# Optimization experiments

Hardware: AMD Instinct MI355X
Metric: run time of the kernel (lower is better)

The kernel has to match this reference:

```python
import jax, jax.numpy as jnp
import numpy as np

# Problem dims: batch B, n variables, m constraints (from A_shape=(512,256))
B, N, M_CON = 64, 256, 512
# OSQP ADMM hyper-parameters (standard OSQP defaults: sigma, rho, relaxation alpha)
SIGMA, RHO, ALPHA = 1e-6, 0.1, 1.6
ITERS = 200  # fixed iteration count (max_iter) for jit-compatibility


def setup_inputs() -> dict:
    key = jax.random.key(0)
    k1, k2, k3, k4, k5 = jax.random.split(key, 5)
    # Diagonal PSD P: strictly positive diagonal values
    P_val = jax.random.uniform(k1, (B, N), dtype=jnp.float32) + 0.1
    q_val = jax.random.normal(k2, (B, N), dtype=jnp.float32)
    # Dense A, row-major flattened [m*n]; scaled for conditioning
    A_val = jax.random.normal(k3, (B, M_CON * N), dtype=jnp.float32) * 0.1
    # Bounds with l < 0 < u roughly (x=0 feasible -> QP always solvable)
    c = jax.random.normal(k4, (B, M_CON), dtype=jnp.float32)
    w = jax.random.uniform(k5, (B, M_CON), dtype=jnp.float32)
    l_val = c - w - 0.1
    u_val = c + w + 0.1
    return {"P_val": P_val, "q_val": q_val, "A_val": A_val,
            "l_val": l_val, "u_val": u_val}


def _cho_solve(L, rhs):
    # batched lower-triangular Cholesky solve: M x = rhs, M = L L^T
    y = jax.scipy.linalg.solve_triangular(L, rhs[..., None], lower=True)
    x = jax.scipy.linalg.solve_triangular(jnp.swapaxes(L, -1, -2), y, lower=False)
    return x[..., 0]


def _osqp_admm(P_diag, q, A, l, u):
    """Batched OSQP ADMM: min 1/2 x'Px + q'x  s.t. l <= Ax <= u.
    P is diagonal (P_diag per-item diagonal). Returns primal solution x [B, n]."""
    n = q.shape[-1]
    # KKT-condensed matrix: M = P + sigma*I + rho*A'A, Cholesky-factored once.
    Mmat = jax.vmap(jnp.diag)(P_diag) + SIGMA * jnp.eye(n, dtype=q.dtype) \
        + RHO * jnp.einsum('bmi,bmj->bij', A, A)
    L = jnp.linalg.cholesky(Mmat)

    def step(carry, _):
        x, z, y = carry
        rhs = SIGMA * x - q + jnp.einsum('bmn,bm->bn', A, RHO * z - y)
        x_tilde = _cho_solve(L, rhs)                  # [B, n]
        z_tilde = jnp.einsum('bmn,bn->bm', A, x_tilde)  # [B, m]
        x_new = ALPHA * x_tilde + (1.0 - ALPHA) * x
        z_relax = ALPHA * z_tilde + (1.0 - ALPHA) * z
        z_new = jnp.clip(z_relax + y / RHO, l, u)     # projection onto [l, u]
        y_new = y + RHO * (z_relax - z_new)
        return (x_new, z_new, y_new), None

    init = (jnp.zeros_like(q), jnp.zeros_like(l), jnp.zeros_like(l))
    (x, _, _), _ = jax.lax.scan(step, init, None, length=ITERS)
    return x


def reference(P_val, q_val, A_val, l_val, u_val):
    A = A_val.reshape(B, M_CON, N)
    return _osqp_admm(P_val, q_val, A, l_val, u_val)
```

## Files before the change

### kernel.cpp

```cpp
#include <hip/hip_runtime.h>
#include <hip/hip_fp16.h>

#define B_      64
#define N_      256
#define M_      512
#define SIGMA_  1e-6f
#define RHO_    0.1f
#define ALPHA_  1.6f
#define BETA_   (-0.6f)
#define ITERS_  200

#if defined(__has_builtin)
#if __has_builtin(__builtin_amdgcn_fdot2)
#define HAVE_FDOT2 1
#endif
#endif

typedef _Float16 h2_t __attribute__((ext_vector_type(2)));

__device__ __forceinline__ float fdot2f(__half2 a, __half2 b, float c) {
#ifdef HAVE_FDOT2
    return __builtin_amdgcn_fdot2(__builtin_bit_cast(h2_t, a),
                                  __builtin_bit_cast(h2_t, b), c, false);
#else
    return c + __low2float(a) * __low2float(b) + __high2float(a) * __high2float(b);
#endif
}

__device__ __forceinline__ float fdot2u(unsigned int a, unsigned int b, float c) {
    return fdot2f(__builtin_bit_cast(__half2, a), __builtin_bit_cast(__half2, b), c);
}

__device__ __forceinline__ unsigned short bf16rne(float f) {
    unsigned int u = __builtin_bit_cast(unsigned int, f);
    u += 0x7fffu + ((u >> 16) & 1u);
    return (unsigned short)(u >> 16);
}
__device__ __forceinline__ float bf16tof(unsigned short h) {
    unsigned int u = ((unsigned int)h) << 16;
    return __builtin_bit_cast(float, u);
}

__device__ __forceinline__ float f4c(const float4& v, int k) {
    return k == 0 ? v.x : k == 1 ? v.y : k == 2 ? v.z : v.w;
}

__global__ __launch_bounds__(256) void gemm_bt(
    const float* __restrict__ Af, const __half* __restrict__ Ah, int lda, long long sA, int tA,
    const float* __restrict__ Bf, int ldb, long long sB, int tB,
    const float* __restrict__ Dp, int ldd, long long sD,
    float* __restrict__ Cf, __half* __restrict__ Ch, int ldc, long long sC,
    float alpha, float beta, int Mx, int Nx, int Kx, int packPairs,
    float* __restrict__ Gdr, long long sGdr)
{
    __shared__ float as_[16][68];
    __shared__ float bs_[16][68];

    const int tid = threadIdx.x;
    const int b   = blockIdx.z;
    const int i0  = blockIdx.y * 64;
    const int j0  = blockIdx.x * 64;

    if (Af) Af += (size_t)b * sA;
    if (Ah) Ah += (size_t)b * sA;
    Bf += (size_t)b * sB;
    if (Dp) Dp += (size_t)b * sD;
    if (Cf) Cf += (size_t)b * sC;
    if (Ch) Ch += (size_t)b * sC;
    if (Gdr) Gdr += (size_t)b * sGdr;

    const int ty = tid >> 4;
    const int tx = tid & 15;

    float acc[4][4] = {};

    #pragma unroll 1
    for (int k0 = 0; k0 < Kx; k0 += 16) {
        if (tA) {
            const int kk = tid >> 4, i4 = (tid & 15) << 2;
            float4 v = *(const float4*)(Af + (size_t)(k0 + kk) * lda + i0 + i4);
            *(float4*)&as_[kk][i4] = v;
        } else {
            const int ii = tid >> 2, k4 = (tid & 3) << 2;
            if (Ah) {
                const __half2* hp = (const __half2*)(Ah + (size_t)(i0 + ii) * lda + k0 + k4);
                __half2 h0 = hp[0], h1 = hp[1];
                as_[k4 + 0][ii] = __low2float(h0);
                as_[k4 + 1][ii] = __high2float(h0);
                as_[k4 + 2][ii] = __low2float(h1);
                as_[k4 + 3][ii] = __high2float(h1);
            } else {
                float4 v = *(const float4*)(Af + (size_t)(i0 + ii) * lda + k0 + k4);
                as_[k4 + 0][ii] = v.x; as_[k4 + 1][ii] = v.y;
                as_[k4 + 2][ii] = v.z; as_[k4 + 3][ii] = v.w;
            }
        }
        if (tB) {
            const int jj = tid >> 2, k4 = (tid & 3) << 2;
            float4 v = *(const float4*)(Bf + (size_t)(j0 + jj) * ldb + k0 + k4);
            bs_[k4 + 0][jj] = v.x; bs_[k4 + 1][jj] = v.y;
            bs_[k4 + 2][jj] = v.z; bs_[k4 + 3][jj] = v.w;
        } else {
            const int kk = tid >> 4, j4 = (tid & 15) << 2;
            float4 v = *(const float4*)(Bf + (size_t)(k0 + kk) * ldb + j0 + j4);
            *(float4*)&bs_[kk][j4] = v;
        }
        __syncthreads();

        #pragma unroll
        for (int kk = 0; kk < 16; kk++) {
            float4 av = *(float4*)&as_[kk][ty << 2];
            float4 bv = *(float4*)&bs_[kk][tx << 2];
            acc[0][0] += av.x * bv.x; acc[0][1] += av.x * bv.y;
            acc[0][2] += av.x * bv.z; acc[0][3] += av.x * bv.w;
            acc[1][0] += av.y * bv.x; acc[1][1] += av.y * bv.y;
            acc[1][2] += av.y * bv.z; acc[1][3] += av.y * bv.w;
            acc[2][0] += av.z * bv.x; acc[2][1] += av.z * bv.y;
            acc[2][2] += av.z * bv.z; acc[2][3] += av.z * bv.w;
            acc[3][0] += av.w * bv.x; acc[3][1] += av.w * bv.y;
            acc[3][2] += av.w * bv.z; acc[3][3] += av.w * bv.w;
        }
        __syncthreads();
    }

    if (Ch) {
        if (packPairs) {
            __half2* C2 = (__half2*)Ch;
            const int mrow = i0 + (ty << 2);
            #pragma unroll
            for (int p = 0; p < 2; p++) {
                #pragma unroll
                for (int jj = 0; jj < 4; jj++) {
                    const float v0 = alpha * acc[2 * p][jj];
                    const float v1 = alpha * acc[2 * p + 1][jj];
                    __half2 h = __floats2half2_rn(v0, v1);
                    C2[(size_t)((mrow >> 1) + p) * ldc + j0 + (tx << 2) + jj] = h;
                    if (Gdr) {
                        const int col = j0 + (tx << 2) + jj;
                        const int r0  = mrow + 2 * p;
                        if (col == r0)          Gdr[col] = v0 - __low2float(h);
                        else if (col == r0 + 1) Gdr[col] = v1 - __high2float(h);
                    }
                }
            }
        } else {
            #pragma unroll
            for (int ii = 0; ii < 4; ii++) {
                #pragma unroll
                for (int jj = 0; jj < 4; jj++) {
                    Ch[(size_t)(i0 + (ty << 2) + ii) * ldc + j0 + (tx << 2) + jj] =
                        __float2half_rn(alpha * acc[ii][jj]);
                }
            }
        }
    } else {
        #pragma unroll
        for (int ii = 0; ii < 4; ii++) {
            const int m = i0 + (ty << 2) + ii;
            const int n = j0 + (tx << 2);
            float4 v;
            v.x = alpha * acc[ii][0]; v.y = alpha * acc[ii][1];
            v.z = alpha * acc[ii][2]; v.w = alpha * acc[ii][3];
            if (Dp) {
                float4 d = *(const float4*)(Dp + (size_t)m * ldd + n);
                v.x += beta * d.x; v.y += beta * d.y;
                v.z += beta * d.z; v.w += beta * d.w;
            }
            *(float4*)(Cf + (size_t)m * ldc + n) = v;
        }
    }
}

typedef __attribute__((ext_vector_type(8))) short bfrag;
typedef __attribute__((ext_vector_type(4))) float ffrag;

__global__ __launch_bounds__(256) void mfma_nt(
    const unsigned short* __restrict__ Xh, const unsigned short* __restrict__ Xl,
    const unsigned short* __restrict__ Yh, const unsigned short* __restrict__ Yl,
    int Kx, long long sX, long long sY,
    void* __restrict__ out0, void* __restrict__ out1,
    int ldc, long long sC, long long sC2, int mode,
    const float* __restrict__ Pd, float alpha)
{
    __shared__ unsigned short Ysh[2][64][264];

    const int tid = threadIdx.x;
    const int w   = tid >> 6;
    const int l   = tid & 63;
    const int b   = blockIdx.z;
    const int rowbase = blockIdx.y * 64 + w * 16;
    const int colbase = blockIdx.x * 64;
    const int lr = l & 15;
    const int q  = l >> 4;

    const unsigned short* xh = Xh + (size_t)b * sX + (size_t)(rowbase + lr) * Kx + q * 8;
    const unsigned short* xl = Xl + (size_t)b * sX + (size_t)(rowbase + lr) * Kx + q * 8;
    const unsigned short* ybh = Yh + (size_t)b * sY;
    const unsigned short* ybl = Yl + (size_t)b * sY;

    ffrag acc[4] = {};

    #pragma unroll 1
    for (int kc = 0; kc < Kx; kc += 256) {
        __syncthreads();
        #pragma unroll
        for (int e = 0; e < 8; e++) {
            const int idx = e * 256 + tid;
            const int c  = idx >> 5;
            const int kq = idx & 31;
            const size_t so = (size_t)(colbase + c) * Kx + kc + kq * 8;
            *(uint4*)&Ysh[0][c][kq * 8] = *(const uint4*)(ybh + so);
            *(uint4*)&Ysh[1][c][kq * 8] = *(const uint4*)(ybl + so);
        }
        __syncthreads();

        #pragma unroll 2
        for (int k0 = kc; k0 < kc + 256; k0 += 32) {
            bfrag ah = *(const bfrag*)(xh + k0);
            bfrag al = *(const bfrag*)(xl + k0);
            const int ko = (k0 - kc) + q * 8;
            #pragma unroll
            for (int t = 0; t < 4; t++) {
                bfrag bh = *(const bfrag*)&Ysh[0][16 * t + lr][ko];
                bfrag bl = *(const bfrag*)&Ysh[1][16 * t + lr][ko];
                acc[t] = __builtin_amdgcn_mfma_f32_16x16x32_bf16(ah, bh, acc[t], 0, 0, 0);
                acc[t] = __builtin_amdgcn_mfma_f32_16x16x32_bf16(ah, bl, acc[t], 0, 0, 0);
                acc[t] = __builtin_amdgcn_mfma_f32_16x16x32_bf16(al, bh, acc[t], 0, 0, 0);
            }
        }
    }

    if (mode == 0) {
        float* Cf = (float*)out0 + (size_t)b * sC;
        #pragma unroll
        for (int t = 0; t < 4; t++) {
            #pragma unroll
            for (int p = 0; p < 4; p++) {
                const int r  = rowbase + q * 4 + p;
                const int cc = colbase + 16 * t + lr;
                float v = alpha * acc[t][p];
                if (Pd && cc == r) v += Pd[b * 256 + r] + SIGMA_;
                Cf[(size_t)r * ldc + cc] = v;
            }
        }
    } else if (mode == 1) {
        unsigned short* Fh = (unsigned short*)out0 + (size_t)b * sC;
        unsigned short* Fl = (unsigned short*)out1 + (size_t)b * sC;
        #pragma unroll
        for (int t = 0; t < 4; t++) {
            #pragma unroll
            for (int p = 0; p < 4; p++) {
                const int r  = rowbase + q * 4 + p;
                const int cc = colbase + 16 * t + lr;
                const float v = acc[t][p];
                const unsigned short hh = bf16rne(v);
                Fh[(size_t)r * ldc + cc] = hh;
                Fl[(size_t)r * ldc + cc] = bf16rne(v - bf16tof(hh));
            }
        }
    } else {
        unsigned int* Gpp = (unsigned int*)out0 + (size_t)b * sC;
        float* Gd = (float*)out1 + (size_t)b * sC2;
        #pragma unroll
        for (int t = 0; t < 4; t++) {
            #pragma unroll
            for (int p2 = 0; p2 < 2; p2++) {
                const int r0 = rowbase + q * 4 + 2 * p2;
                const int cc = colbase + 16 * t + lr;
                const float v0 = acc[t][2 * p2], v1 = acc[t][2 * p2 + 1];
                __half2 h = __floats2half2_rn(v0, v1);
                Gpp[(size_t)(r0 >> 1) * ldc + cc] = __builtin_bit_cast(unsigned int, h);
                if (cc == r0)          Gd[cc] = v0 - __low2float(h);
                else if (cc == r0 + 1) Gd[cc] = v1 - __high2float(h);
            }
        }
    }
}

__global__ __launch_bounds__(256) void prep_a(
    const float* __restrict__ A, unsigned short* __restrict__ Th,
    unsigned short* __restrict__ Tl, unsigned short* __restrict__ Ahh,
    unsigned short* __restrict__ All)
{
    __shared__ float t_[64][65];
    const int b  = blockIdx.z;
    const int r0 = blockIdx.x * 64;
    const int c0 = blockIdx.y * 64;
    const int tid = threadIdx.x;
    const int ty = tid >> 4, tx = tid & 15;
    const float* Ab = A + (size_t)b * 131072;
    unsigned short* Ahb = Ahh + (size_t)b * 131072;
    unsigned short* Alb = All + (size_t)b * 131072;

    #pragma unroll
    for (int p = 0; p < 4; p++) {
        const int rr = ty + p * 16;
        const size_t o = (size_t)(r0 + rr) * 256 + c0 + tx * 4;
        float4 v = *(const float4*)(Ab + o);
        t_[rr][tx * 4 + 0] = v.x; t_[rr][tx * 4 + 1] = v.y;
        t_[rr][tx * 4 + 2] = v.z; t_[rr][tx * 4 + 3] = v.w;
        unsigned short h0 = bf16rne(v.x), h1 = bf16rne(v.y);
        unsigned short h2 = bf16rne(v.z), h3 = bf16rne(v.w);
        uint2 hp, lp;
        hp.x = (unsigned int)h0 | ((unsigned int)h1 << 16);
        hp.y = (unsigned int)h2 | ((unsigned int)h3 << 16);
        lp.x = (unsigned int)bf16rne(v.x - bf16tof(h0)) |
               ((unsigned int)bf16rne(v.y - bf16tof(h1)) << 16);
        lp.y = (unsigned int)bf16rne(v.z - bf16tof(h2)) |
               ((unsigned int)bf16rne(v.w - bf16tof(h3)) << 16);
        *(uint2*)(Ahb + o) = hp;
        *(uint2*)(Alb + o) = lp;
    }
    __syncthreads();

    unsigned short* Thb = Th + (size_t)b * 131072;
    unsigned short* Tlb = Tl + (size_t)b * 131072;
    #pragma unroll
    for (int p = 0; p < 4; p++) {
        const int ar = ty + p * 16;
        unsigned int hp[2], lp[2];
        #pragma unroll
        for (int d2 = 0; d2 < 2; d2++) {
            unsigned short h0, h1, l0, l1;
            {
                const float v = t_[tx * 4 + 2 * d2][ar];
                h0 = bf16rne(v); l0 = bf16rne(v - bf16tof(h0));
            }
            {
                const float v = t_[tx * 4 + 2 * d2 + 1][ar];
                h1 = bf16rne(v); l1 = bf16rne(v - bf16tof(h1));
            }
            hp[d2] = (unsigned int)h0 | ((unsigned int)h1 << 16);
            lp[d2] = (unsigned int)l0 | ((unsigned int)l1 << 16);
        }
        const size_t o = (size_t)(c0 + ar) * 512 + r0 + tx * 4;
        *(uint2*)(Thb + o) = make_uint2(hp[0], hp[1]);
        *(uint2*)(Tlb + o) = make_uint2(lp[0], lp[1]);
    }
}

__global__ void add_diag(float* __restrict__ Mm, const float* __restrict__ P)
{
    const int b = blockIdx.x, t = threadIdx.x;
    Mm[(size_t)b * 65536 + (size_t)t * 257] += P[b * 256 + t] + SIGMA_;
}

__device__ __forceinline__ int gja(int i, int j)
{
    return (i << 7) + ((((j >> 2) ^ (i & 31)) << 2) | (j & 3));
}
__device__ __forceinline__ float4 ldsq(const float* Mp, int row, int q)
{
    return *(const float4*)&Mp[(row << 7) + (((q ^ (row & 31)) << 2))];
}
__device__ __forceinline__ void stsq(float* Mp, int row, int q, float4 v)
{
    *(float4*)&Mp[(row << 7) + (((q ^ (row & 31)) << 2))] = v;
}

__device__ void gj_lds(float* Msh, float (&Dsh)[16][17], float (&CT)[16][136],
                       float (&RS)[16][136], float (&CDs)[16][136],
                       float (&rowB)[2][16], float (&colB)[2][16], float (&pB)[2],
                       int tid)
{
    const int di = tid >> 4;
    const int dj = tid & 15;

    #pragma unroll 1
    for (int t = 0; t < 8; t++) {
        const int tb = t << 4;

        float a = Msh[gja(tb + di, tb + dj)];
        #pragma unroll
        for (int g2 = 0; g2 < 2; g2++) {
            const int i0 = (dj << 2) + (g2 << 6);
            float4 cv;
            if ((i0 >> 4) == t) {
                cv.x = 0.f; cv.y = 0.f; cv.z = 0.f; cv.w = 0.f;
            } else {
                cv.x = Msh[gja(i0 + 0, tb + di)];
                cv.y = Msh[gja(i0 + 1, tb + di)];
                cv.z = Msh[gja(i0 + 2, tb + di)];
                cv.w = Msh[gja(i0 + 3, tb + di)];
            }
            *(float4*)&CT[di][i0] = cv;
        }
        __syncthreads();

        #pragma unroll 1
        for (int k = 0; k < 16; k++) {
            const int kb = k & 1;
            if (dj == k) colB[kb][di] = a;
            if (di == k) {
                rowB[kb][dj] = a;
                if (dj == k) pB[kb] = 1.0f / a;
            }
            __syncthreads();
            const float ip = pB[kb];
            const float rj = rowB[kb][dj];
            const float ci = colB[kb][di];
            if (di == k)      a = (dj == k) ? ip : rj * ip;
            else if (dj == k) a = -ci * ip;
            else              a -= ci * (rj * ip);
        }
        Dsh[di][dj] = a;
        __syncthreads();

        #pragma unroll
        for (int g2 = 0; g2 < 2; g2++) {
            const int j = (dj << 2) + (g2 << 6);
            float4 s; s.x = 0.f; s.y = 0.f; s.z = 0.f; s.w = 0.f;
            if ((j >> 4) != t) {
                #pragma unroll
                for (int m = 0; m < 16; m++) {
                    const float d = Dsh[di][m];
                    const float4 rv = ldsq(Msh, tb + m, j >> 2);
                    s.x += d * rv.x; s.y += d * rv.y;
                    s.z += d * rv.z; s.w += d * rv.w;
                }
            }
            *(float4*)&RS[di][j] = s;

            float4 sc; sc.x = 0.f; sc.y = 0.f; sc.z = 0.f; sc.w = 0.f;
            #pragma unroll
            for (int m = 0; m < 16; m++) {
                const float d = Dsh[m][di];
                const float4 cv = *(const float4*)&CT[m][j];
                sc.x += d * cv.x; sc.y += d * cv.y;
                sc.z += d * cv.z; sc.w += d * cv.w;
            }
            *(float4*)&CDs[di][j] = sc;
        }
        __syncthreads();

        {
            const int ty = di, tx = dj;
            float4 v0[8], v1[8];
            int cofs0[8], cofs1[8];
            #pragma unroll
            for (int r = 0; r < 8; r++) {
                const int i = (ty << 3) + r;
                const int e = i & 31;
                const int base = i << 7;
                cofs0[r] = base + ((((tx << 1)     ) ^ e) << 2);
                cofs1[r] = base + ((((tx << 1) | 1 ) ^ e) << 2);
                v0[r] = *(float4*)&Msh[cofs0[r]];
                v1[r] = *(float4*)&Msh[cofs1[r]];
            }
            #pragma unroll 1
            for (int k = 0; k < 16; k++) {
                const float4 r0 = *(const float4*)&RS[k][tx << 3];
                const float4 r1 = *(const float4*)&RS[k][(tx << 3) + 4];
                const float4 c0 = *(const float4*)&CT[k][ty << 3];
                const float4 c1 = *(const float4*)&CT[k][(ty << 3) + 4];
                const float cc[8] = {c0.x, c0.y, c0.z, c0.w,
                                     c1.x, c1.y, c1.z, c1.w};
                #pragma unroll
                for (int r = 0; r < 8; r++) {
                    const float c = cc[r];
                    v0[r].x -= c * r0.x; v0[r].y -= c * r0.y;
                    v0[r].z -= c * r0.z; v0[r].w -= c * r0.w;
                    v1[r].x -= c * r1.x; v1[r].y -= c * r1.y;
                    v1[r].z -= c * r1.z; v1[r].w -= c * r1.w;
                }
            }
            #pragma unroll
            for (int r = 0; r < 8; r++) {
                *(float4*)&Msh[cofs0[r]] = v0[r];
                *(float4*)&Msh[cofs1[r]] = v1[r];
            }
        }
        __syncthreads();

        #pragma unroll
        for (int g2 = 0; g2 < 2; g2++) {
            const int j = (dj << 2) + (g2 << 6);
            if ((j >> 4) != t) {
                stsq(Msh, tb + di, j >> 2, *(const float4*)&RS[di][j]);
                const float4 cd = *(const float4*)&CDs[di][j];
                Msh[gja(j + 0, tb + di)] = -cd.x;
                Msh[gja(j + 1, tb + di)] = -cd.y;
                Msh[gja(j + 2, tb + di)] = -cd.z;
                Msh[gja(j + 3, tb + di)] = -cd.w;
            }
        }
        Msh[gja(tb + di, tb + dj)] = Dsh[di][dj];
        __syncthreads();
    }
}

__global__ __launch_bounds__(256) void gj128_blk(
    const float* __restrict__ src, int lsrc, long long ssrc,
    float* __restrict__ dst, int ldst, long long sdst)
{
    extern __shared__ float Msh[];
    __shared__ float Dsh[16][17];
    __shared__ float CT[16][136];
    __shared__ float RS[16][136];
    __shared__ float CDs[16][136];
    __shared__ float rowB[2][16], colB[2][16], pB[2];

    const int tid = threadIdx.x, b = blockIdx.x;
    src += (size_t)b * ssrc;
    dst += (size_t)b * sdst;

    for (int qd = 0; qd < 64; qd++) {
        const int idx = qd * 256 + tid;
        const int i = idx >> 7, j = idx & 127;
        Msh[gja(i, j)] = src[(size_t)i * lsrc + j];
    }
    __syncthreads();
    gj_lds(Msh, Dsh, CT, RS, CDs, rowB, colB, pB, tid);
    for (int qd = 0; qd < 64; qd++) {
        const int idx = qd * 256 + tid;
        const int i = idx >> 7, j = idx & 127;
        dst[(size_t)i * ldst + j] = Msh[gja(i, j)];
    }
}

__global__ __launch_bounds__(256) void schur_inv(
    const float* __restrict__ Mmat, float* __restrict__ Ebuf,
    float* __restrict__ Minv, unsigned short* __restrict__ Mh,
    unsigned short* __restrict__ Ml)
{
    __shared__ float A1[16384];
    __shared__ float A2[16384];
    __shared__ float Dsh[16][17];
    __shared__ float CT[16][136];
    __shared__ float RS[16][136];
    __shared__ float CDs[16][136];
    __shared__ float rowB[2][16], colB[2][16], pB[2];

    const int tid = threadIdx.x, b = blockIdx.x;
    const float* Mb = Mmat + (size_t)b * 65536;
    float* Eb = Ebuf + (size_t)b * 16384;
    float* Ib = Minv + (size_t)b * 65536;
    unsigned short* Mhb = Mh + (size_t)b * 65536;
    unsigned short* Mlb = Ml + (size_t)b * 65536;

    const int ty = tid >> 4, tx = tid & 15;

    for (int qd = 0; qd < 64; qd++) {
        const int idx = qd * 256 + tid;
        const int i = idx >> 7, j = idx & 127;
        A1[gja(i, j)] = Mb[(size_t)i * 256 + j];
    }
    __syncthreads();
    gj_lds(A1, Dsh, CT, RS, CDs, rowB, colB, pB, tid);

    for (int qd = 0; qd < 64; qd++) {
        const int idx = qd * 256 + tid;
        const int i = idx >> 7, j = idx & 127;
        Eb[(size_t)i * 128 + j] = A1[gja(i, j)];
        A2[gja(i, j)] = Mb[(size_t)(128 + i) * 256 + j];
    }
    __syncthreads();

    {
        float acc[8][8] = {};
        #pragma unroll 1
        for (int k4 = 0; k4 < 32; k4++) {
            float4 mq[8];
            #pragma unroll
            for (int r = 0; r < 8; r++) mq[r] = ldsq(A2, 8 * ty + r, k4);
            #pragma unroll
            for (int kk = 0; kk < 4; kk++) {
                const int k = k4 * 4 + kk;
                const float4 e0 = ldsq(A1, k, 2 * tx);
                const float4 e1 = ldsq(A1, k, 2 * tx + 1);
                const float ev[8] = {e0.x, e0.y, e0.z, e0.w, e1.x, e1.y, e1.z, e1.w};
                #pragma unroll
                for (int r = 0; r < 8; r++) {
                    const float m = f4c(mq[r], kk);
                    #pragma unroll
                    for (int c = 0; c < 8; c++) acc[r][c] += m * ev[c];
                }
            }
        }
        __syncthreads();
        #pragma unroll
        for (int r = 0; r < 8; r++) {
            float4 o0, o1;
            o0.x = acc[r][0]; o0.y = acc[r][1]; o0.z = acc[r][2]; o0.w = acc[r][3];
            o1.x = acc[r][4]; o1.y = acc[r][5]; o1.z = acc[r][6]; o1.w = acc[r][7];
            stsq(A2, 8 * ty + r, 2 * tx, o0);
            stsq(A2, 8 * ty + r, 2 * tx + 1, o1);
        }
        __syncthreads();
    }

    {
        float acc[8][8];
        #pragma unroll
        for (int r = 0; r < 8; r++) {
            const float4 a0 = *(const float4*)&Mb[(size_t)(128 + 8 * ty + r) * 256 + 128 + 8 * tx];
            const float4 a1 = *(const float4*)&Mb[(size_t)(128 + 8 * ty + r) * 256 + 128 + 8 * tx + 4];
            acc[r][0] = a0.x; acc[r][1] = a0.y; acc[r][2] = a0.z; acc[r][3] = a0.w;
            acc[r][4] = a1.x; acc[r][5] = a1.y; acc[r][6] = a1.z; acc[r][7] = a1.w;
        }
        #pragma unroll 1
        for (int kt = 0; kt < 8; kt++) {
            __syncthreads();
            #pragma unroll
            for (int e = 0; e < 8; e++) {
                const int idx = e * 256 + tid;
                const int kk = idx >> 7, j = idx & 127;
                RS[kk][j] = Mb[(size_t)(kt * 16 + kk) * 256 + 128 + j];
            }
            __syncthreads();
            #pragma unroll 1
            for (int k2 = 0; k2 < 16; k2 += 4) {
                const int kq = (kt * 16 + k2) >> 2;
                float4 tq[8];
                #pragma unroll
                for (int r = 0; r < 8; r++) tq[r] = ldsq(A2, 8 * ty + r, kq);
                #pragma unroll
                for (int kk = 0; kk < 4; kk++) {
                    const float4 m0 = *(const float4*)&RS[k2 + kk][8 * tx];
                    const float4 m1 = *(const float4*)&RS[k2 + kk][8 * tx + 4];
                    const float mv[8] = {m0.x, m0.y, m0.z, m0.w, m1.x, m1.y, m1.z, m1.w};
                    #pragma unroll
                    for (int r = 0; r < 8; r++) {
                        const float t2 = f4c(tq[r], kk);
                        #pragma unroll
                        for (int c = 0; c < 8; c++) acc[r][c] -= t2 * mv[c];
                    }
                }
            }
        }
        __syncthreads();
        #pragma unroll
        for (int r = 0; r < 8; r++) {
            float4 o0, o1;
            o0.x = acc[r][0]; o0.y = acc[r][1]; o0.z = acc[r][2]; o0.w = acc[r][3];
            o1.x = acc[r][4]; o1.y = acc[r][5]; o1.z = acc[r][6]; o1.w = acc[r][7];
            stsq(A1, 8 * ty + r, 2 * tx, o0);
            stsq(A1, 8 * ty + r, 2 * tx + 1, o1);
        }
        __syncthreads();
    }

    gj_lds(A1, Dsh, CT, RS, CDs, rowB, colB, pB, tid);
    for (int qd = 0; qd < 64; qd++) {
        const int idx = qd * 256 + tid;
        const int i = idx >> 7, j = idx & 127;
        const float v = A1[gja(i, j)];
        const size_t o = (size_t)(128 + i) * 256 + 128 + j;
        Ib[o] = v;
        const unsigned short hh = bf16rne(v);
        Mhb[o] = hh; Mlb[o] = bf16rne(v - bf16tof(hh));
    }

    {
        float acc[8][8] = {};
        #pragma unroll 1
        for (int k4 = 0; k4 < 32; k4++) {
            float4 sq[8];
            #pragma unroll
            for (int r = 0; r < 8; r++) sq[r] = ldsq(A1, 8 * ty + r, k4);
            #pragma unroll
            for (int kk = 0; kk < 4; kk++) {
                const int k = k4 * 4 + kk;
                const float4 t0 = ldsq(A2, k, 2 * tx);
                const float4 t1 = ldsq(A2, k, 2 * tx + 1);
                const float tv[8] = {t0.x, t0.y, t0.z, t0.w, t1.x, t1.y, t1.z, t1.w};
                #pragma unroll
                for (int r = 0; r < 8; r++) {
                    const float m = f4c(sq[r], kk);
                    #pragma unroll
                    for (int c = 0; c < 8; c++) acc[r][c] += m * tv[c];
                }
            }
        }
        __syncthreads();
        #pragma unroll
        for (int r = 0; r < 8; r++) {
            float4 o0, o1;
            o0.x = acc[r][0]; o0.y = acc[r][1]; o0.z = acc[r][2]; o0.w = acc[r][3];
            o1.x = acc[r][4]; o1.y = acc[r][5]; o1.z = acc[r][6]; o1.w = acc[r][7];
            stsq(A1, 8 * ty + r, 2 * tx, o0);
            stsq(A1, 8 * ty + r, 2 * tx + 1, o1);
        }
        __syncthreads();
    }

    for (int qd = 0; qd < 64; qd++) {
        const int idx = qd * 256 + tid;
        const int i = idx >> 7, j = idx & 127;
        const float v = -A1[gja(i, j)];
        const size_t o = (size_t)(128 + i) * 256 + j;
        Ib[o] = v;
        const unsigned short hh = bf16rne(v);
        Mhb[o] = hh; Mlb[o] = bf16rne(v - bf16tof(hh));
    }
    for (int qd = 0; qd < 64; qd++) {
        const int idx = qd * 256 + tid;
        const int j = idx >> 7, i = idx & 127;
        const float v = -A1[gja(i, j)];
        const size_t o = (size_t)j * 256 + 128 + i;
        Ib[o] = v;
        const unsigned short hh = bf16rne(v);
        Mhb[o] = hh; Mlb[o] = bf16rne(v - bf16tof(hh));
    }

    {
        float acc[8][8] = {};
        #pragma unroll 1
        for (int k = 0; k < 128; k++) {
            const float4 t0 = ldsq(A2, k, 2 * ty);
            const float4 t1 = ldsq(A2, k, 2 * ty + 1);
            const float4 v0 = ldsq(A1, k, 2 * tx);
            const float4 v1 = ldsq(A1, k, 2 * tx + 1);
            const float tv[8] = {t0.x, t0.y, t0.z, t0.w, t1.x, t1.y, t1.z, t1.w};
            const float vv[8] = {v0.x, v0.y, v0.z, v0.w, v1.x, v1.y, v1.z, v1.w};
            #pragma unroll
            for (int r = 0; r < 8; r++)
                #pragma unroll
                for (int c = 0; c < 8; c++) acc[r][c] += tv[r] * vv[c];
        }
        #pragma unroll
        for (int r = 0; r < 8; r++) {
            const float4 e0 = *(const float4*)&Eb[(size_t)(8 * ty + r) * 128 + 8 * tx];
            const float4 e1 = *(const float4*)&Eb[(size_t)(8 * ty + r) * 128 + 8 * tx + 4];
            const float ev[8] = {e0.x, e0.y, e0.z, e0.w, e1.x, e1.y, e1.z, e1.w};
            #pragma unroll
            for (int c = 0; c < 8; c++) {
                const float v = acc[r][c] + ev[c];
                const size_t o = (size_t)(8 * ty + r) * 256 + 8 * tx + c;
                Ib[o] = v;
                const unsigned short hh = bf16rne(v);
                Mhb[o] = hh; Mlb[o] = bf16rne(v - bf16tof(hh));
            }
        }
    }
}

__global__ void assemble_offdiag(float* __restrict__ Minv, const float* __restrict__ V)
{
    const int b = blockIdx.x, tid = threadIdx.x;
    const float* Vb = V + (size_t)b * 16384;
    float* Mb = Minv + (size_t)b * 65536;
    for (int qd = 0; qd < 64; qd++) {
        const int idx = qd * 256 + tid;
        const int i = idx >> 7, j = idx & 127;
        const float v = -Vb[idx];
        Mb[(size_t)(128 + i) * 256 + j] = v;
        Mb[(size_t)j * 256 + 128 + i]   = v;
    }
}

__global__ __launch_bounds__(512) void c0d0_kernel(
    const float* __restrict__ Minv, const float* __restrict__ q,
    const float* __restrict__ A, float* __restrict__ c0, float* __restrict__ d0)
{
    __shared__ float qs[256], c0s[256];
    const int b = blockIdx.x, tid = threadIdx.x;
    const float* Mb = Minv + (size_t)b * 65536;

    if (tid < 256) qs[tid] = q[b * 256 + tid];
    __syncthreads();
    if (tid < 256) {
        float acc = 0.f;
        for (int j = 0; j < 256; j++)
            acc += Mb[(size_t)j * 256 + tid] * qs[j];
        c0s[tid] = -acc;
        c0[b * 256 + tid] = -acc;
    }
    __syncthreads();

    const int wid = tid >> 6, lane = tid & 63;
    const float* Ab = A + (size_t)b * 131072;
    for (int m = wid; m < 512; m += 8) {
        float4 a4 = *(const float4*)(Ab + (size_t)m * 256 + (lane << 2));
        float4 c4 = *(const float4*)&c0s[lane << 2];
        float acc = a4.x * c4.x + a4.y * c4.y + a4.z * c4.z + a4.w * c4.w;
        for (int off = 32; off > 0; off >>= 1) acc += __shfl_down(acc, off, 64);
        if (lane == 0) d0[b * 512 + m] = acc;
    }
}

__global__ __launch_bounds__(512, 2) void solver_reg(
    const unsigned int* __restrict__ Gp,
    const float* __restrict__ Gdr,
    const float* __restrict__ d0g,
    const float* __restrict__ lg, const float* __restrict__ ug,
    float* __restrict__ uout)
{
    __shared__ unsigned int Gsh[16384];
    __shared__ float part[4][512];
    __shared__ unsigned int rp_sh[256];

    const int tid = threadIdx.x;
    const int b   = blockIdx.x;
    const int g   = tid >> 7;
    const int iq  = tid & 127;

    const unsigned int* Gb = Gp + (size_t)b * 131072;

    {
        const uint4* src4 = (const uint4*)Gb;
        uint4* dst4 = (uint4*)Gsh;
        #pragma unroll
        for (int n = 0; n < 8; n++)
            dst4[n * 512 + tid] = src4[n * 512 + tid];
    }

    const uint4* gb4 = (const uint4*)Gb + (size_t)(32 + 56 * g) * 128 + iq;
    uint4 gc[56];
    #pragma unroll
    for (int d = 0; d < 56; d++) gc[d] = gb4[(size_t)d * 128];

    const float d0v  = d0g[b * 512 + tid];
    const float lv   = lg[b * 512 + tid];
    const float uv   = ug[b * 512 + tid];
    const float gdrv = Gdr[b * 512 + tid];
    float z = 0.f, y = 0.f, ua = 0.f;

    const unsigned int* lbase = Gsh + (g << 12) + (iq << 2);

    __syncthreads();

    #pragma unroll 1
    for (int it = 0; it < ITERS_; it++) {
        const float rv = RHO_ * z - y;
        ua = BETA_ * ua + ALPHA_ * rv;
        const float rv2 = __shfl_xor(rv, 1);
        if (!(tid & 1))
            rp_sh[tid >> 1] =
                __builtin_bit_cast(unsigned int, __floats2half2_rn(rv, rv2));
        __syncthreads();

        float a0 = 0.f, a1 = 0.f, a2 = 0.f, a3 = 0.f;
        #pragma unroll
        for (int k = 0; k < 8; k++) {
            uint4 gv = *(const uint4*)(lbase + (k << 9));
            const unsigned int r = rp_sh[(g << 3) + k];
            a0 = fdot2u(gv.x, r, a0); a1 = fdot2u(gv.y, r, a1);
            a2 = fdot2u(gv.z, r, a2); a3 = fdot2u(gv.w, r, a3);
        }
        #pragma unroll
        for (int k = 0; k < 56; k++) {
            const unsigned int r = rp_sh[32 + 56 * g + k];
            a0 = fdot2u(gc[k].x, r, a0); a1 = fdot2u(gc[k].y, r, a1);
            a2 = fdot2u(gc[k].z, r, a2); a3 = fdot2u(gc[k].w, r, a3);
        }
        {
            float4 pv; pv.x = a0; pv.y = a1; pv.z = a2; pv.w = a3;
            *(float4*)&part[g][iq << 2] = pv;
        }
        __syncthreads();

        float sum = part[0][tid] + part[1][tid] + part[2][tid] + part[3][tid];
        const float rv_ = RHO_ * z - y;
        const float zt = d0v + sum + gdrv * rv_;
        const float zr = ALPHA_ * zt + (1.0f - ALPHA_) * z;
        const float w  = zr + y * (1.0f / RHO_);
        const float zn = fminf(fmaxf(w, lv), uv);
        y = RHO_ * (w - zn);
        z = zn;
    }

    uout[b * 512 + tid] = ua;
}

__global__ __launch_bounds__(256) void finalx(
    const float* __restrict__ Minv, const float* __restrict__ c0,
    const float* __restrict__ uacc, const float* __restrict__ A,
    float* __restrict__ out)
{
    __shared__ float us2[512], t1s[256];
    const int b = blockIdx.x, tid = threadIdx.x;

    us2[tid]       = uacc[b * 512 + tid];
    us2[tid + 256] = uacc[b * 512 + 256 + tid];
    __syncthreads();

    const float* Ab = A + (size_t)b * 131072;
    float acc = 0.f;
    for (int m = 0; m < 512; m++)
        acc += Ab[(size_t)m * 256 + tid] * us2[m];
    t1s[tid] = acc;
    __syncthreads();

    const float* Mb = Minv + (size_t)b * 65536;
    float x = c0[b * 256 + tid];
    for (int j = 0; j < 256; j++)
        x += Mb[(size_t)j * 256 + tid] * t1s[j];
    out[b * 256 + tid] = x;
}

__global__ __launch_bounds__(256) void finalx_split(
    const unsigned short* __restrict__ Mh, const unsigned short* __restrict__ Ml,
    const float* __restrict__ c0, const float* __restrict__ uacc,
    const float* __restrict__ A, float* __restrict__ out)
{
    __shared__ float us2[512], t1s[256];
    const int b = blockIdx.x, tid = threadIdx.x;

    us2[tid]       = uacc[b * 512 + tid];
    us2[tid + 256] = uacc[b * 512 + 256 + tid];
    __syncthreads();

    const float* Ab = A + (size_t)b * 131072;
    float acc = 0.f;
    for (int m = 0; m < 512; m++)
        acc += Ab[(size_t)m * 256 + tid] * us2[m];
    t1s[tid] = acc;
    __syncthreads();

    const unsigned short* Mhb = Mh + (size_t)b * 65536;
    const unsigned short* Mlb = Ml + (size_t)b * 65536;
    float x = c0[b * 256 + tid];
    for (int j = 0; j < 256; j++) {
        const float m = bf16tof(Mhb[(size_t)j * 256 + tid]) +
                        bf16tof(Mlb[(size_t)j * 256 + tid]);
        x += m * t1s[j];
    }
    out[b * 256 + tid] = x;
}

extern "C" void kernel_launch(void* const* d_in, const int* in_sizes, int n_in,
                              void* d_out, int out_size, void* d_ws, size_t ws_size,
                              hipStream_t stream)
{
    (void)in_sizes; (void)n_in; (void)out_size;

    const float* P = (const float*)d_in[0];
    const float* q = (const float*)d_in[1];
    const float* A = (const float*)d_in[2];
    const float* l = (const float*)d_in[3];
    const float* u = (const float*)d_in[4];
    float* out = (float*)d_out;
    char* ws = (char*)d_ws;

    (void)hipFuncSetAttribute(reinterpret_cast<const void*>(&gj128_blk),
                              hipFuncAttributeMaxDynamicSharedMemorySize, 65536);

    const bool fullPath = (ws_size >= (161ull << 20));

    if (fullPath) {
        float*  Mmat = (float*)(ws);
        float*  Minv = (float*)(ws + (16ull << 20));
        float*  Ebuf = (float*)(ws + (32ull << 20));
        unsigned short* Mh  = (unsigned short*)(ws + (48ull << 20));
        unsigned short* Ml  = (unsigned short*)(ws + (56ull << 20));
        unsigned short* Ahh = (unsigned short*)(ws + (64ull << 20));
        unsigned short* All = (unsigned short*)(ws + (80ull << 20));
        unsigned short* Fhh = (unsigned short*)(ws + (96ull << 20));
        unsigned short* Fll = (unsigned short*)(ws + (112ull << 20));
        unsigned int*   G   = (unsigned int*)(ws + (128ull << 20));
        char* tail = ws + (160ull << 20);
        float* c0  = (float*)(tail);
        float* d0  = (float*)(tail + 65536);
        float* ua  = (float*)(tail + 196608);
        float* Gdr = (float*)(tail + 327680);

        prep_a<<<dim3(8, 4, 64), 256, 0, stream>>>(A, Fhh, Fll, Ahh, All);

        mfma_nt<<<dim3(4, 4, 64), 256, 0, stream>>>(
            Fhh, Fll, Fhh, Fll, 512, 131072, 131072,
            (void*)Mmat, nullptr, 256, 65536, 0, 0, P, RHO_);

        schur_inv<<<64, 256, 0, stream>>>(Mmat, Ebuf, Minv, Mh, Ml);

        c0d0_kernel<<<64, 512, 0, stream>>>(Minv, q, A, c0, d0);

        mfma_nt<<<dim3(4, 8, 64), 256, 0, stream>>>(
            Ahh, All, Mh, Ml, 256, 131072, 65536,
            (void*)Fhh, (void*)Fll, 256, 131072, 0, 1, nullptr, 1.f);

        mfma_nt<<<dim3(8, 8, 64), 256, 0, stream>>>(
            Fhh, Fll, Ahh, All, 256, 131072, 131072,
            (void*)G, (void*)Gdr, 512, 131072, 512, 2, nullptr, 1.f);

        solver_reg<<<64, 512, 0, stream>>>(G, Gdr, d0, l, u, ua);

        finalx_split<<<64, 256, 0, stream>>>(Mh, Ml, c0, ua, A, out);
    } else {
        float*  Mmat = (float*)(ws);
        __half* Fh   = (__half*)(ws);
        float*  Minv = (float*)(ws + (16ull << 20));
        float*  E    = (float*)(ws + (32ull << 20));
        float*  T    = (float*)(ws + (36ull << 20));
        float*  S    = (float*)(ws + (40ull << 20));
        float*  V    = (float*)(ws + (44ull << 20));
        __half* G    = (__half*)(ws + (32ull << 20));
        char*   tail = ws + (64ull << 20);
        float*  c0   = (float*)(tail);
        float*  d0   = (float*)(tail + 65536);
        float*  ua   = (float*)(tail + 196608);
        float*  Gdr  = (float*)(tail + 327680);

        gemm_bt<<<dim3(4, 4, 64), 256, 0, stream>>>(
            A, nullptr, 256, 131072, 1,  A, 256, 131072, 0,
            nullptr, 0, 0,  Mmat, nullptr, 256, 65536,
            RHO_, 0.f, 256, 256, 512, 0, nullptr, 0);
        add_diag<<<64, 256, 0, stream>>>(Mmat, P);
        gj128_blk<<<64, 256, 65536, stream>>>(Mmat, 256, 65536, E, 128, 16384);
        gemm_bt<<<dim3(2, 2, 64), 256, 0, stream>>>(
            Mmat + 128 * 256, nullptr, 256, 65536, 0,  E, 128, 16384, 0,
            nullptr, 0, 0,  T, nullptr, 128, 16384,
            1.f, 0.f, 128, 128, 128, 0, nullptr, 0);
        gemm_bt<<<dim3(2, 2, 64), 256, 0, stream>>>(
            T, nullptr, 128, 16384, 0,  Mmat + 128, 256, 65536, 0,
            Mmat + 128 * 256 + 128, 256, 65536,
            S, nullptr, 128, 16384,
            -1.f, 1.f, 128, 128, 128, 0, nullptr, 0);
        gj128_blk<<<64, 256, 65536, stream>>>(S, 128, 16384, Minv + 128 * 256 + 128, 256, 65536);
        gemm_bt<<<dim3(2, 2, 64), 256, 0, stream>>>(
            Minv + 128 * 256 + 128, nullptr, 256, 65536, 0,  T, 128, 16384, 0,
            nullptr, 0, 0,  V, nullptr, 128, 16384,
            1.f, 0.f, 128, 128, 128, 0, nullptr, 0);
        gemm_bt<<<dim3(2, 2, 64), 256, 0, stream>>>(
            T, nullptr, 128, 16384, 1,  V, 128, 16384, 0,
            E, 128, 16384,
            Minv, nullptr, 256, 65536,
            1.f, 1.f, 128, 128, 128, 0, nullptr, 0);
        assemble_offdiag<<<64, 256, 0, stream>>>(Minv, V);
        c0d0_kernel<<<64, 512, 0, stream>>>(Minv, q, A, c0, d0);
        gemm_bt<<<dim3(4, 8, 64), 256, 0, stream>>>(
            A, nullptr, 256, 131072, 0,  Minv, 256, 65536, 0,
            nullptr, 0, 0,  nullptr, Fh, 256, 131072,
            1.f, 0.f, 512, 256, 256, 0, nullptr, 0);
        gemm_bt<<<dim3(8, 8, 64), 256, 0, stream>>>(
            nullptr, Fh, 256, 131072, 0,  A, 256, 131072, 1,
            nullptr, 0, 0,  nullptr, G, 512, 262144,
            1.f, 0.f, 512, 512, 256, 1, Gdr, 512);
        solver_reg<<<64, 512, 0, stream>>>((const unsigned int*)G, Gdr, d0, l, u, ua);
        finalx<<<64, 256, 0, stream>>>(Minv, c0, ua, A, out);
    }
}
```

Measured before the change: 862.4 us.

## Restructure ADMM solver loop to 256 threads with two constraints each, one barrier

The iterative solver kernel changes from 512 threads, each owning one constraint and a quarter of the reduction, to 256 threads that each own two constraint rows and do the full dot product. This drops the partial-sum shared buffer and the second barrier per iteration, and double-buffers the packed residual vector so one barrier per iteration is enough. More of G is cached in LDS and the rest sits in 416 registers per thread. The cost is fewer threads and heavy register pressure, which could cause spills, plus a longer serial dot product per thread.

```diff
diff --git a/kernel.cpp b/kernel.cpp
--- a/kernel.cpp
+++ b/kernel.cpp
@@ -779,21 +779,18 @@
     }
 }
 
-__global__ __launch_bounds__(512, 2) void solver_reg(
+__global__ __launch_bounds__(256, 1) void solver_2c(
     const unsigned int* __restrict__ Gp,
     const float* __restrict__ Gdr,
     const float* __restrict__ d0g,
     const float* __restrict__ lg, const float* __restrict__ ug,
     float* __restrict__ uout)
 {
-    __shared__ unsigned int Gsh[16384];
-    __shared__ float part[4][512];
-    __shared__ unsigned int rp_sh[256];
+    __shared__ unsigned int Gsh[24576];
+    __shared__ unsigned int rp_sh[2][256];
 
     const int tid = threadIdx.x;
     const int b   = blockIdx.x;
-    const int g   = tid >> 7;
-    const int iq  = tid & 127;
 
     const unsigned int* Gb = Gp + (size_t)b * 131072;
 
@@ -801,66 +798,82 @@
         const uint4* src4 = (const uint4*)Gb;
         uint4* dst4 = (uint4*)Gsh;
         #pragma unroll
-        for (int n = 0; n < 8; n++)
-            dst4[n * 512 + tid] = src4[n * 512 + tid];
-    }
-
-    const uint4* gb4 = (const uint4*)Gb + (size_t)(32 + 56 * g) * 128 + iq;
-    uint4 gc[56];
+        for (int n = 0; n < 24; n++)
+            dst4[n * 256 + tid] = src4[n * 256 + tid];
+    }
+
+    const uint2* gb2 = (const uint2*)Gb + (size_t)48 * 256 + tid;
+    uint2 gc[208];
     #pragma unroll
-    for (int d = 0; d < 56; d++) gc[d] = gb4[(size_t)d * 128];
-
-    const float d0v  = d0g[b * 512 + tid];
-    const float lv   = lg[b * 512 + tid];
-    const float uv   = ug[b * 512 + tid];
-    const float gdrv = Gdr[b * 512 + tid];
-    float z = 0.f, y = 0.f, ua = 0.f;
-
-    const unsigned int* lbase = Gsh + (g << 12) + (iq << 2);
+    for (int d = 0; d < 208; d++) gc[d] = gb2[(size_t)d * 256];
+
+    const float2 d0v  = *(const float2*)&d0g[b * 512 + 2 * tid];
+    const float2 lv   = *(const float2*)&lg[b * 512 + 2 * tid];
+    const float2 uv   = *(const float2*)&ug[b * 512 + 2 * tid];
+    const float2 gdrv = *(const float2*)&Gdr[b * 512 + 2 * tid];
+    float z0 = 0.f, z1 = 0.f, y0 = 0.f, y1 = 0.f, ua0 = 0.f, ua1 = 0.f;
+
+    const unsigned int* lbase = Gsh + 2 * tid;
 
     __syncthreads();
 
     #pragma unroll 1
     for (int it = 0; it < ITERS_; it++) {
-        const float rv = RHO_ * z - y;
-        ua = BETA_ * ua + ALPHA_ * rv;
-        const float rv2 = __shfl_xor(rv, 1);
-        if (!(tid & 1))
-            rp_sh[tid >> 1] =
-                __builtin_bit_cast(unsigned int, __floats2half2_rn(rv, rv2));
-        __syncthreads();
-
-        float a0 = 0.f, a1 = 0.f, a2 = 0.f, a3 = 0.f;
-        #pragma unroll
-        for (int k = 0; k < 8; k++) {
-            uint4 gv = *(const uint4*)(lbase + (k << 9));
-            const unsigned int r = rp_sh[(g << 3) + k];
-            a0 = fdot2u(gv.x, r, a0); a1 = fdot2u(gv.y, r, a1);
-            a2 = fdot2u(gv.z, r, a2); a3 = fdot2u(gv.w, r, a3);
-        }
-        #pragma unroll
-        for (int k = 0; k < 56; k++) {
-            const unsigned int r = rp_sh[32 + 56 * g + k];
-            a0 = fdot2u(gc[k].x, r, a0); a1 = fdot2u(gc[k].y, r, a1);
-            a2 = fdot2u(gc[k].z, r, a2); a3 = fdot2u(gc[k].w, r, a3);
-        }
+        const float rv0 = RHO_ * z0 - y0;
+        const float rv1 = RHO_ * z1 - y1;
+        ua0 = BETA_ * ua0 + ALPHA_ * rv0;
+        ua1 = BETA_ * ua1 + ALPHA_ * rv1;
+        unsigned int* rp = rp_sh[it & 1];
+        rp[tid] = __builtin_bit_cast(unsigned int, __floats2half2_rn(rv0, rv1));
+        __syncthreads();
+
+        float a00 = 0.f, a01 = 0.f, a10 = 0.f, a11 = 0.f;
+        #pragma unroll
+        for (int j4 = 0; j4 < 12; j4++) {
+            uint4 rr = *(const uint4*)&rp[j4 << 2];
+            #pragma unroll
+            for (int d = 0; d < 4; d++) {
+                const int jj = (j4 << 2) + d;
+                uint2 g = *(const uint2*)(lbase + (jj << 9));
+                const unsigned int r =
+                    d == 0 ? rr.x : d == 1 ? rr.y : d == 2 ? rr.z : rr.w;
+                if (d & 1) { a01 = fdot2u(g.x, r, a01); a11 = fdot2u(g.y, r, a11); }
+                else       { a00 = fdot2u(g.x, r, a00); a10 = fdot2u(g.y, r, a10); }
+            }
+        }
+        #pragma unroll
+        for (int k4 = 0; k4 < 52; k4++) {
+            uint4 rr = *(const uint4*)&rp[48 / 4 * 4 + (k4 << 2)];
+            #pragma unroll
+            for (int d = 0; d < 4; d++) {
+                const uint2 g = gc[(k4 << 2) + d];
+                const unsigned int r =
+                    d == 0 ? rr.x : d == 1 ? rr.y : d == 2 ? rr.z : rr.w;
+                if (d & 1) { a01 = fdot2u(g.x, r, a01); a11 = fdot2u(g.y, r, a11); }
+                else       { a00 = fdot2u(g.x, r, a00); a10 = fdot2u(g.y, r, a10); }
+            }
+        }
+
         {
-            float4 pv; pv.x = a0; pv.y = a1; pv.z = a2; pv.w = a3;
-            *(float4*)&part[g][iq << 2] = pv;
-        }
-        __syncthreads();
-
-        float sum = part[0][tid] + part[1][tid] + part[2][tid] + part[3][tid];
-        const float rv_ = RHO_ * z - y;
-        const float zt = d0v + sum + gdrv * rv_;
-        const float zr = ALPHA_ * zt + (1.0f - ALPHA_) * z;
-        const float w  = zr + y * (1.0f / RHO_);
-        const float zn = fminf(fmaxf(w, lv), uv);
-        y = RHO_ * (w - zn);
-        z = zn;
-    }
-
-    uout[b * 512 + tid] = ua;
+            const float zt = d0v.x + (a00 + a01) + gdrv.x * rv0;
+            const float zr = ALPHA_ * zt + (1.0f - ALPHA_) * z0;
+            const float w  = zr + y0 * (1.0f / RHO_);
+            const float zn = fminf(fmaxf(w, lv.x), uv.x);
+            y0 = RHO_ * (w - zn);
+            z0 = zn;
+        }
+        {
+            const float zt = d0v.y + (a10 + a11) + gdrv.y * rv1;
+            const float zr = ALPHA_ * zt + (1.0f - ALPHA_) * z1;
+            const float w  = zr + y1 * (1.0f / RHO_);
+            const float zn = fminf(fmaxf(w, lv.y), uv.y);
+            y1 = RHO_ * (w - zn);
+            z1 = zn;
+        }
+    }
+
+    float2 uo; uo.x = ua0; uo.y = ua1;
+    *(float2*)&uout[b * 512 + 2 * tid] = uo;
 }
 
 __global__ __launch_bounds__(256) void finalx(
@@ -973,7 +986,7 @@
             Fhh, Fll, Ahh, All, 256, 131072, 131072,
             (void*)G, (void*)Gdr, 512, 131072, 512, 2, nullptr, 1.f);
 
-        solver_reg<<<64, 512, 0, stream>>>(G, Gdr, d0, l, u, ua);
+        solver_2c<<<64, 256, 0, stream>>>(G, Gdr, d0, l, u, ua);
 
         finalx_split<<<64, 256, 0, stream>>>(Mh, Ml, c0, ua, A, out);
     } else {
@@ -1026,7 +1039,7 @@
             nullptr, Fh, 256, 131072, 0,  A, 256, 131072, 1,
             nullptr, 0, 0,  nullptr, G, 512, 262144,
             1.f, 0.f, 512, 512, 256, 1, Gdr, 512);
-        solver_reg<<<64, 512, 0, stream>>>((const unsigned int*)G, Gdr, d0, l, u, ua);
+        solver_2c<<<64, 256, 0, stream>>>((const unsigned int*)G, Gdr, d0, l, u, ua);
         finalx<<<64, 256, 0, stream>>>(Minv, c0, ua, A, out);
     }
 }
```

New measurement: 1.300 ms. 1.51x slower.
